# Performance work log

Measured on AMD Instinct MI355X. Metric: run time of the kernel, lower is better.

The kernel has to match this reference:

```python
import jax, jax.numpy as jnp
import numpy as np

N = 50000   # nodes
E = 200000  # edges
C = 32      # conv_dim
ND = 75     # n_atom_features
ED = 12     # n_bond_features
L = 3       # num_layer
G = 500     # num graphs in batch
HID = 5     # neurons_message
EPS = 1e-5


def leaky(v):
    return jnp.where(v > 0, v, 0.01 * v)


def setup_inputs() -> dict:
    key = jax.random.key(0)
    ks = jax.random.split(key, 16)
    x = jax.random.normal(ks[0], (N, ND), jnp.float32)
    edge_index = jax.random.randint(ks[1], (2, E), 0, N, jnp.int32)
    edge_attr = jax.random.uniform(ks[2], (E, ED), jnp.float32)
    batch = jnp.sort(jax.random.randint(ks[3], (N,), 0, G, jnp.int32))
    return {
        "x": x,
        "edge_index": edge_index,
        "edge_attr": edge_attr,
        "batch": batch,
        "lin_W": jax.random.normal(ks[4], (ND, C), jnp.float32) * 0.1,
        "lin_b": jnp.zeros((C,), jnp.float32),
        "mes_W1": jax.random.normal(ks[5], (L, ED, HID), jnp.float32) * 0.3,
        "mes_b1": jnp.zeros((L, HID), jnp.float32),
        "mes_W2": jax.random.normal(ks[6], (L, HID, C * C), jnp.float32) * 0.05,
        "mes_b2": jnp.zeros((L, C * C), jnp.float32),
        "root_W": jax.random.normal(ks[7], (L, C, C), jnp.float32) * 0.1,
        "conv_b": jnp.zeros((L, C), jnp.float32),
        "bn_g": jnp.ones((L, C), jnp.float32),
        "bn_b": jnp.zeros((L, C), jnp.float32),
        "pred_W": jax.random.normal(ks[8], (C, 1), jnp.float32) * 0.1,
        "pred_b": jnp.zeros((1,), jnp.float32),
    }


def reference(x, edge_index, edge_attr, batch, lin_W, lin_b, mes_W1, mes_b1,
              mes_W2, mes_b2, root_W, conv_b, bn_g, bn_b, pred_W, pred_b):
    src, dst = edge_index[0], edge_index[1]
    # initial atom projection
    h = leaky(x @ lin_W + lin_b)  # [N, C]
    for l in range(L):
        # edge MLP -> per-edge weight matrix [E, C, C]
        w = jnp.maximum(edge_attr @ mes_W1[l] + mes_b1[l], 0.0)
        w = (w @ mes_W2[l] + mes_b2[l]).reshape(E, C, C)
        # gather source features, per-edge matmul, scatter-add to targets
        msg = jnp.einsum('ec,ecd->ed', h[src], w)  # [E, C]
        agg = jax.ops.segment_sum(msg, dst, num_segments=N)  # [N, C]
        out = agg + h @ root_W[l] + conv_b[l]
        # batch norm (batch statistics over nodes)
        mu = out.mean(axis=0)
        var = out.var(axis=0)
        out = (out - mu) / jnp.sqrt(var + EPS) * bn_g[l] + bn_b[l]
        if l < L - 1:
            out = leaky(out)
        h = out  # JK == 'last'
    # graph readout: scatter_add over batch ids, then prediction head
    g = jax.ops.segment_sum(h, batch, num_segments=G)  # [G, C]
    return g @ pred_W + pred_b  # [G, 1]
```

## Files before the change

### kernel.cpp

```cpp
#include <hip/hip_runtime.h>

namespace {

constexpr int kN = 50000, kE = 200000, kG = 500;
constexpr float kEps = 1e-5f;

typedef short v8s __attribute__((ext_vector_type(8)));
typedef float v4f __attribute__((ext_vector_type(4)));

__device__ __forceinline__ unsigned short bf16rn(float x) {
    unsigned u = __float_as_uint(x);
    return (unsigned short)((u + 0x7FFFu + ((u >> 16) & 1u)) >> 16);
}
__device__ __forceinline__ float bf16lo(unsigned p) { return __uint_as_float(p << 16); }
__device__ __forceinline__ float bf16hi(unsigned p) { return __uint_as_float(p & 0xFFFF0000u); }
__device__ __forceinline__ unsigned pk2(float a, float b) {
    return (unsigned)bf16rn(a) | ((unsigned)bf16rn(b) << 16);
}

__global__ __launch_bounds__(1024) void init_h(
    const float* __restrict__ x, const float* __restrict__ W,
    const float* __restrict__ b, unsigned short* __restrict__ h16)
{
    __shared__ unsigned short sx[256 * 96];
    __shared__ unsigned short sW[32 * 96];
    int t = threadIdx.x;
    for (int i = t; i < 256 * 96; i += 1024) sx[i] = 0;
    for (int i = t; i < 32 * 96; i += 1024) sW[i] = 0;
    __syncthreads();
    int tb = blockIdx.x * 256;
    int cnt = min(256, kN - tb);
    for (int i = t; i < cnt * 75; i += 1024) {
        int n = i / 75, f = i - n * 75;
        sx[n * 96 + f] = bf16rn(x[(size_t)tb * 75 + i]);
    }
    for (int i = t; i < 75 * 32; i += 1024) {
        int f = i >> 5, c = i & 31;
        sW[c * 96 + f] = bf16rn(W[i]);
    }
    __syncthreads();
    int l15 = t & 15, quad = (t >> 4) & 3, w = t >> 6;
    int n = tb + w * 16 + l15;
    unsigned* H = (unsigned*)h16;
    #pragma unroll
    for (int tile = 0; tile < 2; ++tile) {
        v4f acc = {0.f, 0.f, 0.f, 0.f};
        #pragma unroll
        for (int kc = 0; kc < 3; ++kc) {
            v8s a  = *(const v8s*)&sW[(tile * 16 + l15) * 96 + kc * 32 + quad * 8];
            v8s bb = *(const v8s*)&sx[(w * 16 + l15) * 96 + kc * 32 + quad * 8];
            acc = __builtin_amdgcn_mfma_f32_16x16x32_bf16(a, bb, acc, 0, 0, 0);
        }
        if (n < kN) {
            int c0 = tile * 16 + quad * 4;
            float v0 = acc[0] + b[c0],     v1 = acc[1] + b[c0 + 1];
            float v2 = acc[2] + b[c0 + 2], v3 = acc[3] + b[c0 + 3];
            v0 = v0 > 0.f ? v0 : 0.01f * v0;  v1 = v1 > 0.f ? v1 : 0.01f * v1;
            v2 = v2 > 0.f ? v2 : 0.01f * v2;  v3 = v3 > 0.f ? v3 : 0.01f * v3;
            H[n * 16 + (c0 >> 1)]     = pk2(v0, v1);
            H[n * 16 + (c0 >> 1) + 1] = pk2(v2, v3);
        }
    }
}

__global__ __launch_bounds__(256) void hid_pre(
    const float* __restrict__ ea, const float* __restrict__ W1,
    const float* __restrict__ b1, unsigned* __restrict__ hidpk)
{
    __shared__ float sE[256 * 13];
    __shared__ float sW[195];
    int t = threadIdx.x;
    for (int i = t; i < 195; i += 256) sW[i] = (i < 180) ? W1[i] : b1[i - 180];
    int base = blockIdx.x * 256;
    int cnt = min(256, kE - base);
    for (int i = t; i < cnt * 12; i += 256) {
        int el = i / 12, f = i - el * 12;
        sE[el * 13 + f] = ea[(size_t)base * 12 + i];
    }
    __syncthreads();
    if (t >= cnt) return;
    int e = base + t;
    float ef[12];
    #pragma unroll
    for (int j = 0; j < 12; ++j) ef[j] = sE[t * 13 + j];
    #pragma unroll
    for (int l = 0; l < 3; ++l) {
        float h[5];
        #pragma unroll
        for (int k = 0; k < 5; ++k) h[k] = sW[180 + l * 5 + k];
        #pragma unroll
        for (int f = 0; f < 12; ++f)
            #pragma unroll
            for (int k = 0; k < 5; ++k)
                h[k] = fmaf(ef[f], sW[l * 60 + f * 5 + k], h[k]);
        #pragma unroll
        for (int k = 0; k < 5; ++k) h[k] = h[k] > 0.f ? h[k] : 0.f;
        size_t o = ((size_t)l * kE + e) * 3;
        hidpk[o + 0] = pk2(h[0], h[1]);
        hidpk[o + 1] = pk2(h[2], h[3]);
        hidpk[o + 2] = pk2(h[4], 0.f);
    }
}

__global__ __launch_bounds__(1024) void y_root(
    const unsigned short* __restrict__ h16, float* __restrict__ obuf,
    const float* __restrict__ W2, const float* __restrict__ b2,
    const float* __restrict__ rW, const float* __restrict__ convb,
    const float* __restrict__ stats,
    const float* __restrict__ gPrev, const float* __restrict__ bPrev,
    int first, unsigned short* __restrict__ Yus)
{
    __shared__ unsigned short sh[256 * 32];
    __shared__ unsigned short sB[256 * 32];
    int t = threadIdx.x;
    int tb = blockIdx.x * 256;
    int cnt = min(256, kN - tb);
    for (int i = t; i < 8192; i += 1024) {
        int co = i >> 5, c = i & 31, d = co >> 3, k = co & 7;
        float v = (k < 5) ? W2[k * 1024 + c * 32 + d]
                : (k == 5) ? b2[c * 32 + d]
                : (k == 6) ? rW[c * 32 + d] : 0.f;
        sB[co * 32 + c] = bf16rn(v);
    }
    if (first) {
        #pragma unroll
        for (int j = 0; j < 8; ++j) {
            int idx = t + j * 1024;
            int nl = idx >> 5, c = idx & 31;
            sh[idx] = (nl < cnt) ? h16[(size_t)(tb + nl) * 32 + c] : (unsigned short)0;
        }
    } else {
        int c = t & 31;
        float mu = stats[c] * (1.f / kN);
        float var = stats[32 + c] * (1.f / kN) - mu * mu;
        float ivg = rsqrtf(var + kEps) * gPrev[c];
        float bb = bPrev[c];
        #pragma unroll
        for (int j = 0; j < 8; ++j) {
            int idx = t + j * 1024;
            int nl = idx >> 5;
            float v = 0.f;
            if (nl < cnt) {
                float o = obuf[(size_t)(tb + nl) * 32 + c];
                v = (o - mu) * ivg + bb;
                v = v > 0.f ? v : 0.01f * v;
            }
            sh[idx] = bf16rn(v);
        }
    }
    __syncthreads();
    int l15 = t & 15, quad = (t >> 4) & 3, w = t >> 6;
    int n = tb + w * 16 + l15;
    v8s bn_ = *(const v8s*)&sh[(w * 16 + l15) * 32 + quad * 8];
    unsigned* Ydw = (unsigned*)Yus;
    #pragma unroll
    for (int i = 0; i < 16; ++i) {
        v8s a = *(const v8s*)&sB[(i * 16 + l15) * 32 + quad * 8];
        v4f acc = {0.f, 0.f, 0.f, 0.f};
        acc = __builtin_amdgcn_mfma_f32_16x16x32_bf16(a, bn_, acc, 0, 0, 0);
        if (n < kN) {
            int cb = i * 16 + quad * 4;
            int d = cb >> 3, koff = cb & 7;
            if (koff == 0) {
                Ydw[(size_t)n * 128 + d * 4]     = pk2(acc[0], acc[1]);
                Ydw[(size_t)n * 128 + d * 4 + 1] = pk2(acc[2], acc[3]);
            } else {
                Ydw[(size_t)n * 128 + d * 4 + 2] = pk2(acc[0], acc[1]);
                obuf[(size_t)n * 32 + d] = acc[2] + convb[d];
            }
        }
    }
}

__global__ __launch_bounds__(256) void edge_msg(
    const int* __restrict__ ei, const unsigned* __restrict__ hp,
    const unsigned short* __restrict__ Yus, float* __restrict__ obuf,
    float* __restrict__ stats)
{
    int t = threadIdx.x;
    if (blockIdx.x == 0 && t < 64) stats[t] = 0.f;
    int gid = blockIdx.x * 256 + t;
    int e = gid >> 5, d = gid & 31;
    int src = ei[e];
    int dst = ei[kE + e];
    unsigned q0 = hp[(size_t)e * 3 + 0];
    unsigned q1 = hp[(size_t)e * 3 + 1];
    unsigned q2 = hp[(size_t)e * 3 + 2];
    uint4 p = *(const uint4*)(Yus + (size_t)src * 256 + d * 8);
    float m = bf16hi(p.z);
    m = fmaf(bf16lo(q0), bf16lo(p.x), m);
    m = fmaf(bf16hi(q0), bf16hi(p.x), m);
    m = fmaf(bf16lo(q1), bf16lo(p.y), m);
    m = fmaf(bf16hi(q1), bf16hi(p.y), m);
    m = fmaf(bf16lo(q2), bf16lo(p.z), m);
    atomicAdd(&obuf[(size_t)dst * 32 + d], m);
}

__global__ __launch_bounds__(256) void bn_reduce(
    const float* __restrict__ obuf, float* __restrict__ stats)
{
    __shared__ float ls[256];
    __shared__ float lq[256];
    int t = threadIdx.x;
    int c = t & 31, row = t >> 5;
    float s = 0.f, q = 0.f;
    for (int n = blockIdx.x * 8 + row; n < kN; n += gridDim.x * 8) {
        float v = obuf[(size_t)n * 32 + c];
        s += v; q += v * v;
    }
    ls[t] = s; lq[t] = q;
    __syncthreads();
    if (t < 128) { ls[t] += ls[t + 128]; lq[t] += lq[t + 128]; }
    __syncthreads();
    if (t < 64) { ls[t] += ls[t + 64]; lq[t] += lq[t + 64]; }
    __syncthreads();
    if (t < 32) {
        atomicAdd(&stats[t], ls[t] + ls[t + 32]);
        atomicAdd(&stats[32 + t], lq[t] + lq[t + 32]);
    }
}

__global__ __launch_bounds__(256) void bn_norm_final(
    const float* __restrict__ obuf, const float* __restrict__ stats,
    const float* __restrict__ g, const float* __restrict__ b,
    float* __restrict__ vbuf, const float* __restrict__ predW,
    float* __restrict__ out, const float* __restrict__ pred_b)
{
    int idx = blockIdx.x * 256 + threadIdx.x;
    if (idx < kG) out[idx] = pred_b[0];
    if (idx >= kN * 32) return;
    int c = idx & 31;
    float mu = stats[c] * (1.f / kN);
    float var = stats[32 + c] * (1.f / kN) - mu * mu;
    float inv = rsqrtf(var + kEps);
    float v = (obuf[idx] - mu) * inv * g[c] + b[c];
    float pv = v * predW[c];
    #pragma unroll
    for (int off = 16; off > 0; off >>= 1) pv += __shfl_down(pv, off, 32);
    if (c == 0) vbuf[idx >> 5] = pv;
}

__global__ __launch_bounds__(256) void seg_readout(
    const float* __restrict__ vbuf, const int* __restrict__ batch,
    float* __restrict__ out)
{
    __shared__ float ls[kG];
    int t = threadIdx.x;
    for (int i = t; i < kG; i += 256) ls[i] = 0.f;
    __syncthreads();
    int base = blockIdx.x * 2048 + t * 8;
    int cur = -1; float acc = 0.f;
    #pragma unroll
    for (int i = 0; i < 8; ++i) {
        int n = base + i;
        if (n >= kN) break;
        int gi = batch[n];
        float val = vbuf[n];
        if (gi != cur) {
            if (cur >= 0) atomicAdd(&ls[cur], acc);
            cur = gi; acc = val;
        } else acc += val;
    }
    if (cur >= 0) atomicAdd(&ls[cur], acc);
    __syncthreads();
    for (int i = t; i < kG; i += 256) {
        float s = ls[i];
        if (s != 0.f) atomicAdd(&out[i], s);
    }
}

}

extern "C" void kernel_launch(void* const* d_in, const int* in_sizes, int n_in,
                              void* d_out, int out_size, void* d_ws, size_t ws_size,
                              hipStream_t stream)
{
    const float* x      = (const float*)d_in[0];
    const int*   ei     = (const int*)d_in[1];
    const float* ea     = (const float*)d_in[2];
    const int*   batch  = (const int*)d_in[3];
    const float* lin_W  = (const float*)d_in[4];
    const float* lin_b  = (const float*)d_in[5];
    const float* mes_W1 = (const float*)d_in[6];
    const float* mes_b1 = (const float*)d_in[7];
    const float* mes_W2 = (const float*)d_in[8];
    const float* mes_b2 = (const float*)d_in[9];
    const float* root_W = (const float*)d_in[10];
    const float* conv_b = (const float*)d_in[11];
    const float* bn_g   = (const float*)d_in[12];
    const float* bn_b   = (const float*)d_in[13];
    const float* pred_W = (const float*)d_in[14];
    const float* pred_b = (const float*)d_in[15];
    float* out = (float*)d_out;

    char* wsb = (char*)d_ws;
    float* stats = (float*)wsb;
    unsigned short* h16 = (unsigned short*)(wsb + 256);
    float* obuf = (float*)(h16 + (size_t)kN * 32);
    unsigned short* Yus = (unsigned short*)(obuf + (size_t)kN * 32);
    unsigned* hidpk = (unsigned*)(Yus + (size_t)kN * 256);
    float* vbuf = (float*)Yus;

    init_h<<<(kN + 255) / 256, 1024, 0, stream>>>(x, lin_W, lin_b, h16);
    hid_pre<<<(kE + 255) / 256, 256, 0, stream>>>(ea, mes_W1, mes_b1, hidpk);

    for (int l = 0; l < 3; ++l) {
        y_root<<<(kN + 255) / 256, 1024, 0, stream>>>(
            h16, obuf, mes_W2 + (size_t)l * 5120, mes_b2 + (size_t)l * 1024,
            root_W + (size_t)l * 1024, conv_b + l * 32, stats,
            bn_g + (l ? (l - 1) * 32 : 0), bn_b + (l ? (l - 1) * 32 : 0),
            l == 0 ? 1 : 0, Yus);
        edge_msg<<<kE * 32 / 256, 256, 0, stream>>>(
            ei, hidpk + (size_t)l * kE * 3, Yus, obuf, stats);
        bn_reduce<<<512, 256, 0, stream>>>(obuf, stats);
    }

    bn_norm_final<<<(kN * 32 + 255) / 256, 256, 0, stream>>>(
        obuf, stats, bn_g + 64, bn_b + 64, vbuf, pred_W, out, pred_b);
    seg_readout<<<(kN + 2047) / 2048, 256, 0, stream>>>(vbuf, batch, out);
}
```

Before: 310.2 us.

## Replace atomic edge scatter with CSR pull aggregation fused with BN statistics

Builds a destination-sorted CSR (degree count, single-block scan, atomic fill) once per call. The per-layer atomic edge_msg scatter and separate bn_reduce pass are replaced by a pull-style agg kernel that sums incoming messages per node and accumulates BN statistics in the same pass. It also switches the per-node Y and h buffers from bf16 to fp32 in a k-major layout and gives each layer its own stats slice. This removes the float atomics and one full obuf read per layer, at the cost of CSR build kernels, a serial single-block scan, doubled Y storage traffic, and load imbalance across node degrees.

```diff
diff --git a/kernel.cpp b/kernel.cpp
--- a/kernel.cpp
+++ b/kernel.cpp
@@ -18,9 +18,16 @@
     return (unsigned)bf16rn(a) | ((unsigned)bf16rn(b) << 16);
 }
 
+__global__ __launch_bounds__(256) void zero_init(int* __restrict__ deg,
+                                                 float* __restrict__ stats) {
+    int i = blockIdx.x * 256 + threadIdx.x;
+    if (i < kN) deg[i] = 0;
+    if (i < 192) stats[i] = 0.f;
+}
+
 __global__ __launch_bounds__(1024) void init_h(
     const float* __restrict__ x, const float* __restrict__ W,
-    const float* __restrict__ b, unsigned short* __restrict__ h16)
+    const float* __restrict__ b, float* __restrict__ hbuf)
 {
     __shared__ unsigned short sx[256 * 96];
     __shared__ unsigned short sW[32 * 96];
@@ -40,32 +47,32 @@
     }
     __syncthreads();
     int l15 = t & 15, quad = (t >> 4) & 3, w = t >> 6;
-    int n = tb + w * 16 + l15;
-    unsigned* H = (unsigned*)h16;
     #pragma unroll
     for (int tile = 0; tile < 2; ++tile) {
         v4f acc = {0.f, 0.f, 0.f, 0.f};
         #pragma unroll
         for (int kc = 0; kc < 3; ++kc) {
-            v8s a  = *(const v8s*)&sW[(tile * 16 + l15) * 96 + kc * 32 + quad * 8];
-            v8s bb = *(const v8s*)&sx[(w * 16 + l15) * 96 + kc * 32 + quad * 8];
+            v8s a  = *(const v8s*)&sx[(w * 16 + l15) * 96 + kc * 32 + quad * 8];
+            v8s bb = *(const v8s*)&sW[(tile * 16 + l15) * 96 + kc * 32 + quad * 8];
             acc = __builtin_amdgcn_mfma_f32_16x16x32_bf16(a, bb, acc, 0, 0, 0);
         }
-        if (n < kN) {
-            int c0 = tile * 16 + quad * 4;
-            float v0 = acc[0] + b[c0],     v1 = acc[1] + b[c0 + 1];
-            float v2 = acc[2] + b[c0 + 2], v3 = acc[3] + b[c0 + 3];
-            v0 = v0 > 0.f ? v0 : 0.01f * v0;  v1 = v1 > 0.f ? v1 : 0.01f * v1;
-            v2 = v2 > 0.f ? v2 : 0.01f * v2;  v3 = v3 > 0.f ? v3 : 0.01f * v3;
-            H[n * 16 + (c0 >> 1)]     = pk2(v0, v1);
-            H[n * 16 + (c0 >> 1) + 1] = pk2(v2, v3);
+        int c = tile * 16 + l15;
+        float bc = b[c];
+        #pragma unroll
+        for (int r = 0; r < 4; ++r) {
+            int n = tb + w * 16 + quad * 4 + r;
+            if (n < kN) {
+                float v = acc[r] + bc;
+                hbuf[(size_t)n * 32 + c] = v > 0.f ? v : 0.01f * v;
+            }
         }
     }
 }
 
 __global__ __launch_bounds__(256) void hid_pre(
     const float* __restrict__ ea, const float* __restrict__ W1,
-    const float* __restrict__ b1, unsigned* __restrict__ hidpk)
+    const float* __restrict__ b1, const int* __restrict__ ei,
+    unsigned* __restrict__ hidpk, int* __restrict__ deg)
 {
     __shared__ float sE[256 * 13];
     __shared__ float sW[195];
@@ -80,6 +87,7 @@
     __syncthreads();
     if (t >= cnt) return;
     int e = base + t;
+    atomicAdd(&deg[ei[kE + e]], 1);
     float ef[12];
     #pragma unroll
     for (int j = 0; j < 12; ++j) ef[j] = sE[t * 13 + j];
@@ -102,24 +110,68 @@
     }
 }
 
+__global__ __launch_bounds__(1024) void csr_scan(
+    const int* __restrict__ deg, int* __restrict__ rowptr,
+    int* __restrict__ cursor)
+{
+    __shared__ int sc[1024];
+    const int C = 49;
+    int t = threadIdx.x;
+    int base = t * C;
+    int s = 0;
+    for (int i = 0; i < C; ++i) {
+        int idx = base + i;
+        if (idx < kN) s += deg[idx];
+    }
+    sc[t] = s;
+    __syncthreads();
+    for (int off = 1; off < 1024; off <<= 1) {
+        int v = (t >= off) ? sc[t - off] : 0;
+        __syncthreads();
+        sc[t] += v;
+        __syncthreads();
+    }
+    int p = sc[t] - s;
+    for (int i = 0; i < C; ++i) {
+        int idx = base + i;
+        if (idx < kN) {
+            rowptr[idx] = p;
+            cursor[idx] = p;
+            p += deg[idx];
+        }
+    }
+    if (t == 1023) rowptr[kN] = p;
+}
+
+__global__ __launch_bounds__(256) void csr_fill(
+    const int* __restrict__ ei, int* __restrict__ cursor,
+    int* __restrict__ csr_src, int* __restrict__ csr_eid)
+{
+    int e = blockIdx.x * 256 + threadIdx.x;
+    if (e >= kE) return;
+    int dst = ei[kE + e];
+    int pos = atomicAdd(&cursor[dst], 1);
+    csr_src[pos] = ei[e];
+    csr_eid[pos] = e;
+}
+
 __global__ __launch_bounds__(1024) void y_root(
-    const unsigned short* __restrict__ h16, float* __restrict__ obuf,
+    const float* __restrict__ hbuf, float* __restrict__ obuf,
     const float* __restrict__ W2, const float* __restrict__ b2,
     const float* __restrict__ rW, const float* __restrict__ convb,
     const float* __restrict__ stats,
     const float* __restrict__ gPrev, const float* __restrict__ bPrev,
-    int first, unsigned short* __restrict__ Yus)
+    int first, float* __restrict__ Yf)
 {
     __shared__ unsigned short sh[256 * 32];
-    __shared__ unsigned short sB[256 * 32];
+    __shared__ unsigned short sB[224 * 32];
     int t = threadIdx.x;
     int tb = blockIdx.x * 256;
     int cnt = min(256, kN - tb);
-    for (int i = t; i < 8192; i += 1024) {
-        int co = i >> 5, c = i & 31, d = co >> 3, k = co & 7;
+    for (int i = t; i < 224 * 32; i += 1024) {
+        int co = i >> 5, c = i & 31, k = co >> 5, d = co & 31;
         float v = (k < 5) ? W2[k * 1024 + c * 32 + d]
-                : (k == 5) ? b2[c * 32 + d]
-                : (k == 6) ? rW[c * 32 + d] : 0.f;
+                : (k == 5) ? b2[c * 32 + d] : rW[c * 32 + d];
         sB[co * 32 + c] = bf16rn(v);
     }
     if (first) {
@@ -127,7 +179,8 @@
         for (int j = 0; j < 8; ++j) {
             int idx = t + j * 1024;
             int nl = idx >> 5, c = idx & 31;
-            sh[idx] = (nl < cnt) ? h16[(size_t)(tb + nl) * 32 + c] : (unsigned short)0;
+            float v = (nl < cnt) ? hbuf[(size_t)(tb + nl) * 32 + c] : 0.f;
+            sh[idx] = bf16rn(v);
         }
     } else {
         int c = t & 31;
@@ -150,64 +203,65 @@
     }
     __syncthreads();
     int l15 = t & 15, quad = (t >> 4) & 3, w = t >> 6;
-    int n = tb + w * 16 + l15;
-    v8s bn_ = *(const v8s*)&sh[(w * 16 + l15) * 32 + quad * 8];
-    unsigned* Ydw = (unsigned*)Yus;
-    #pragma unroll
-    for (int i = 0; i < 16; ++i) {
-        v8s a = *(const v8s*)&sB[(i * 16 + l15) * 32 + quad * 8];
+    v8s a = *(const v8s*)&sh[(w * 16 + l15) * 32 + quad * 8];
+    #pragma unroll
+    for (int i = 0; i < 14; ++i) {
+        v8s bb = *(const v8s*)&sB[(i * 16 + l15) * 32 + quad * 8];
         v4f acc = {0.f, 0.f, 0.f, 0.f};
-        acc = __builtin_amdgcn_mfma_f32_16x16x32_bf16(a, bn_, acc, 0, 0, 0);
-        if (n < kN) {
-            int cb = i * 16 + quad * 4;
-            int d = cb >> 3, koff = cb & 7;
-            if (koff == 0) {
-                Ydw[(size_t)n * 128 + d * 4]     = pk2(acc[0], acc[1]);
-                Ydw[(size_t)n * 128 + d * 4 + 1] = pk2(acc[2], acc[3]);
-            } else {
-                Ydw[(size_t)n * 128 + d * 4 + 2] = pk2(acc[0], acc[1]);
-                obuf[(size_t)n * 32 + d] = acc[2] + convb[d];
+        acc = __builtin_amdgcn_mfma_f32_16x16x32_bf16(a, bb, acc, 0, 0, 0);
+        int co = i * 16 + l15, k = co >> 5, d = co & 31;
+        if (k < 6) {
+            #pragma unroll
+            for (int r = 0; r < 4; ++r) {
+                int n = tb + w * 16 + quad * 4 + r;
+                if (n < kN) Yf[(size_t)n * 192 + k * 32 + d] = acc[r];
             }
-        }
-    }
-}
-
-__global__ __launch_bounds__(256) void edge_msg(
-    const int* __restrict__ ei, const unsigned* __restrict__ hp,
-    const unsigned short* __restrict__ Yus, float* __restrict__ obuf,
-    float* __restrict__ stats)
-{
-    int t = threadIdx.x;
-    if (blockIdx.x == 0 && t < 64) stats[t] = 0.f;
-    int gid = blockIdx.x * 256 + t;
-    int e = gid >> 5, d = gid & 31;
-    int src = ei[e];
-    int dst = ei[kE + e];
-    unsigned q0 = hp[(size_t)e * 3 + 0];
-    unsigned q1 = hp[(size_t)e * 3 + 1];
-    unsigned q2 = hp[(size_t)e * 3 + 2];
-    uint4 p = *(const uint4*)(Yus + (size_t)src * 256 + d * 8);
-    float m = bf16hi(p.z);
-    m = fmaf(bf16lo(q0), bf16lo(p.x), m);
-    m = fmaf(bf16hi(q0), bf16hi(p.x), m);
-    m = fmaf(bf16lo(q1), bf16lo(p.y), m);
-    m = fmaf(bf16hi(q1), bf16hi(p.y), m);
-    m = fmaf(bf16lo(q2), bf16lo(p.z), m);
-    atomicAdd(&obuf[(size_t)dst * 32 + d], m);
-}
-
-__global__ __launch_bounds__(256) void bn_reduce(
-    const float* __restrict__ obuf, float* __restrict__ stats)
-{
+        } else {
+            float cb = convb[d];
+            #pragma unroll
+            for (int r = 0; r < 4; ++r) {
+                int n = tb + w * 16 + quad * 4 + r;
+                if (n < kN) obuf[(size_t)n * 32 + d] = acc[r] + cb;
+            }
+        }
+    }
+}
+
+__global__ __launch_bounds__(256) void agg(
+    const int* __restrict__ rowptr, const int* __restrict__ csr_src,
+    const int* __restrict__ csr_eid, const unsigned* __restrict__ hp,
+    const float* __restrict__ Yf, float* __restrict__ obuf,
+    float* __restrict__ statsL)
+{
+    int t = threadIdx.x;
+    int grp = t >> 5, d = t & 31;
+    int nbase = blockIdx.x * 64 + grp * 8;
+    float s = 0.f, q = 0.f;
+    for (int ii = 0; ii < 8; ++ii) {
+        int n = nbase + ii;
+        if (n >= kN) break;
+        float acc = obuf[(size_t)n * 32 + d];
+        int j0 = rowptr[n], j1 = rowptr[n + 1];
+        for (int j = j0; j < j1; ++j) {
+            int src = csr_src[j];
+            int eid = csr_eid[j];
+            unsigned q0 = hp[(size_t)eid * 3 + 0];
+            unsigned q1 = hp[(size_t)eid * 3 + 1];
+            unsigned q2 = hp[(size_t)eid * 3 + 2];
+            const float* yr = Yf + (size_t)src * 192;
+            float m = yr[160 + d];
+            m = fmaf(bf16lo(q0), yr[d], m);
+            m = fmaf(bf16hi(q0), yr[32 + d], m);
+            m = fmaf(bf16lo(q1), yr[64 + d], m);
+            m = fmaf(bf16hi(q1), yr[96 + d], m);
+            m = fmaf(bf16lo(q2), yr[128 + d], m);
+            acc += m;
+        }
+        obuf[(size_t)n * 32 + d] = acc;
+        s += acc; q += acc * acc;
+    }
     __shared__ float ls[256];
     __shared__ float lq[256];
-    int t = threadIdx.x;
-    int c = t & 31, row = t >> 5;
-    float s = 0.f, q = 0.f;
-    for (int n = blockIdx.x * 8 + row; n < kN; n += gridDim.x * 8) {
-        float v = obuf[(size_t)n * 32 + c];
-        s += v; q += v * v;
-    }
     ls[t] = s; lq[t] = q;
     __syncthreads();
     if (t < 128) { ls[t] += ls[t + 128]; lq[t] += lq[t + 128]; }
@@ -215,8 +269,8 @@
     if (t < 64) { ls[t] += ls[t + 64]; lq[t] += lq[t + 64]; }
     __syncthreads();
     if (t < 32) {
-        atomicAdd(&stats[t], ls[t] + ls[t + 32]);
-        atomicAdd(&stats[32 + t], lq[t] + lq[t + 32]);
+        atomicAdd(&statsL[t], ls[t] + ls[t + 32]);
+        atomicAdd(&statsL[32 + t], lq[t] + lq[t + 32]);
     }
 }
 
@@ -294,28 +348,37 @@
     float* out = (float*)d_out;
 
     char* wsb = (char*)d_ws;
-    float* stats = (float*)wsb;
-    unsigned short* h16 = (unsigned short*)(wsb + 256);
-    float* obuf = (float*)(h16 + (size_t)kN * 32);
-    unsigned short* Yus = (unsigned short*)(obuf + (size_t)kN * 32);
-    unsigned* hidpk = (unsigned*)(Yus + (size_t)kN * 256);
-    float* vbuf = (float*)Yus;
-
-    init_h<<<(kN + 255) / 256, 1024, 0, stream>>>(x, lin_W, lin_b, h16);
-    hid_pre<<<(kE + 255) / 256, 256, 0, stream>>>(ea, mes_W1, mes_b1, hidpk);
+    float* stats   = (float*)wsb;
+    int* deg       = (int*)(wsb + 1024);
+    int* rowptr    = deg + kN;
+    int* cursor    = rowptr + kN + 1;
+    int* csr_src   = cursor + kN;
+    int* csr_eid   = csr_src + kE;
+    float* hbuf    = (float*)(csr_eid + kE);
+    float* obuf    = hbuf + (size_t)kN * 32;
+    float* Yf      = obuf + (size_t)kN * 32;
+    unsigned* hidpk = (unsigned*)(Yf + (size_t)kN * 192);
+    float* vbuf    = Yf;
+
+    zero_init<<<(kN + 255) / 256, 256, 0, stream>>>(deg, stats);
+    init_h<<<(kN + 255) / 256, 1024, 0, stream>>>(x, lin_W, lin_b, hbuf);
+    hid_pre<<<(kE + 255) / 256, 256, 0, stream>>>(ea, mes_W1, mes_b1, ei, hidpk, deg);
+    csr_scan<<<1, 1024, 0, stream>>>(deg, rowptr, cursor);
+    csr_fill<<<(kE + 255) / 256, 256, 0, stream>>>(ei, cursor, csr_src, csr_eid);
 
     for (int l = 0; l < 3; ++l) {
         y_root<<<(kN + 255) / 256, 1024, 0, stream>>>(
-            h16, obuf, mes_W2 + (size_t)l * 5120, mes_b2 + (size_t)l * 1024,
-            root_W + (size_t)l * 1024, conv_b + l * 32, stats,
+            hbuf, obuf, mes_W2 + (size_t)l * 5120, mes_b2 + (size_t)l * 1024,
+            root_W + (size_t)l * 1024, conv_b + l * 32,
+            stats + (l ? (l - 1) * 64 : 0),
             bn_g + (l ? (l - 1) * 32 : 0), bn_b + (l ? (l - 1) * 32 : 0),
-            l == 0 ? 1 : 0, Yus);
-        edge_msg<<<kE * 32 / 256, 256, 0, stream>>>(
-            ei, hidpk + (size_t)l * kE * 3, Yus, obuf, stats);
-        bn_reduce<<<512, 256, 0, stream>>>(obuf, stats);
+            l == 0 ? 1 : 0, Yf);
+        agg<<<(kN + 63) / 64, 256, 0, stream>>>(
+            rowptr, csr_src, csr_eid, hidpk + (size_t)l * kE * 3, Yf, obuf,
+            stats + l * 64);
     }
 
     bn_norm_final<<<(kN * 32 + 255) / 256, 256, 0, stream>>>(
-        obuf, stats, bn_g + 64, bn_b + 64, vbuf, pred_W, out, pred_b);
+        obuf, stats + 128, bn_g + 64, bn_b + 64, vbuf, pred_W, out, pred_b);
     seg_readout<<<(kN + 2047) / 2048, 256, 0, stream>>>(vbuf, batch, out);
 }
```

New measurement: 471.8 us. 52.1% more time.

## Compute edge messages with per-edge MFMA instead of precomputed per-node Y tensor

Applied to the files above, without the earlier changes.

Drops the per-node Y expansion of size N×256 bf16, which every edge then gathered at 512 bytes per edge. Each edge block now gathers only the 64-byte h[src] row and runs MFMAs against the W2/b2 slices in shared memory, weighting the results by the edge hidden activations before atomically scattering to dst. src/dst indices are packed with the hidden values into one uint4 per edge. The BN stat accumulators are spread over 8 replicas per layer to cut atomic contention. The trade is much less memory traffic for more MFMA work per edge and a weight-staging step in every edge block.

```diff
diff --git a/kernel.cpp b/kernel.cpp
--- a/kernel.cpp
+++ b/kernel.cpp
@@ -4,6 +4,8 @@
 
 constexpr int kN = 50000, kE = 200000, kG = 500;
 constexpr float kEps = 1e-5f;
+constexpr int kNB = (kN + 255) / 256;
+constexpr int kEB = (kE + 255) / 256;
 
 typedef short v8s __attribute__((ext_vector_type(8)));
 typedef float v4f __attribute__((ext_vector_type(4)));
@@ -65,7 +67,8 @@
 
 __global__ __launch_bounds__(256) void hid_pre(
     const float* __restrict__ ea, const float* __restrict__ W1,
-    const float* __restrict__ b1, unsigned* __restrict__ hidpk)
+    const float* __restrict__ b1, const int* __restrict__ ei,
+    uint4* __restrict__ hq)
 {
     __shared__ float sE[256 * 13];
     __shared__ float sW[195];
@@ -80,6 +83,8 @@
     __syncthreads();
     if (t >= cnt) return;
     int e = base + t;
+    unsigned src = (unsigned)ei[e];
+    unsigned dst = (unsigned)ei[kE + e];
     float ef[12];
     #pragma unroll
     for (int j = 0; j < 12; ++j) ef[j] = sE[t * 13 + j];
@@ -95,109 +100,153 @@
                 h[k] = fmaf(ef[f], sW[l * 60 + f * 5 + k], h[k]);
         #pragma unroll
         for (int k = 0; k < 5; ++k) h[k] = h[k] > 0.f ? h[k] : 0.f;
-        size_t o = ((size_t)l * kE + e) * 3;
-        hidpk[o + 0] = pk2(h[0], h[1]);
-        hidpk[o + 1] = pk2(h[2], h[3]);
-        hidpk[o + 2] = pk2(h[4], 0.f);
-    }
-}
-
-__global__ __launch_bounds__(1024) void y_root(
-    const unsigned short* __restrict__ h16, float* __restrict__ obuf,
-    const float* __restrict__ W2, const float* __restrict__ b2,
+        hq[(size_t)l * kE + e] = make_uint4(
+            pk2(h[0], h[1]), pk2(h[2], h[3]),
+            (unsigned)bf16rn(h[4]) | (src << 16), dst);
+    }
+}
+
+__global__ __launch_bounds__(256) void norm_root(
+    const float* __restrict__ obuf_prev, unsigned short* __restrict__ h16,
+    float* __restrict__ obuf,
     const float* __restrict__ rW, const float* __restrict__ convb,
-    const float* __restrict__ stats,
+    const float* __restrict__ statsR,
     const float* __restrict__ gPrev, const float* __restrict__ bPrev,
-    int first, unsigned short* __restrict__ Yus)
+    int first)
 {
     __shared__ unsigned short sh[256 * 32];
-    __shared__ unsigned short sB[256 * 32];
+    __shared__ unsigned short sR[32 * 32];
     int t = threadIdx.x;
     int tb = blockIdx.x * 256;
     int cnt = min(256, kN - tb);
-    for (int i = t; i < 8192; i += 1024) {
-        int co = i >> 5, c = i & 31, d = co >> 3, k = co & 7;
-        float v = (k < 5) ? W2[k * 1024 + c * 32 + d]
-                : (k == 5) ? b2[c * 32 + d]
-                : (k == 6) ? rW[c * 32 + d] : 0.f;
-        sB[co * 32 + c] = bf16rn(v);
+    for (int i = t; i < 1024; i += 256) {
+        int d = i >> 5, c = i & 31;
+        sR[d * 32 + c] = bf16rn(rW[c * 32 + d]);
     }
     if (first) {
         #pragma unroll
-        for (int j = 0; j < 8; ++j) {
-            int idx = t + j * 1024;
-            int nl = idx >> 5, c = idx & 31;
-            sh[idx] = (nl < cnt) ? h16[(size_t)(tb + nl) * 32 + c] : (unsigned short)0;
+        for (int j = 0; j < 4; ++j) {
+            int i4 = t + j * 256;
+            int nl = i4 >> 2, part = i4 & 3;
+            uint4 v = make_uint4(0, 0, 0, 0);
+            if (nl < cnt)
+                v = ((const uint4*)(h16 + (size_t)(tb + nl) * 32))[part];
+            ((uint4*)sh)[i4] = v;
         }
     } else {
         int c = t & 31;
-        float mu = stats[c] * (1.f / kN);
-        float var = stats[32 + c] * (1.f / kN) - mu * mu;
+        float sum = 0.f, sq = 0.f;
+        #pragma unroll
+        for (int r = 0; r < 8; ++r) {
+            sum += statsR[r * 64 + c];
+            sq  += statsR[r * 64 + 32 + c];
+        }
+        float mu = sum * (1.f / kN);
+        float var = sq * (1.f / kN) - mu * mu;
         float ivg = rsqrtf(var + kEps) * gPrev[c];
         float bb = bPrev[c];
-        #pragma unroll
-        for (int j = 0; j < 8; ++j) {
-            int idx = t + j * 1024;
+        for (int j = 0; j < 32; ++j) {
+            int idx = t + j * 256;
             int nl = idx >> 5;
             float v = 0.f;
             if (nl < cnt) {
-                float o = obuf[(size_t)(tb + nl) * 32 + c];
+                float o = obuf_prev[(size_t)(tb + nl) * 32 + c];
                 v = (o - mu) * ivg + bb;
                 v = v > 0.f ? v : 0.01f * v;
+                h16[(size_t)(tb + nl) * 32 + c] = bf16rn(v);
             }
             sh[idx] = bf16rn(v);
         }
     }
     __syncthreads();
     int l15 = t & 15, quad = (t >> 4) & 3, w = t >> 6;
-    int n = tb + w * 16 + l15;
-    v8s bn_ = *(const v8s*)&sh[(w * 16 + l15) * 32 + quad * 8];
-    unsigned* Ydw = (unsigned*)Yus;
-    #pragma unroll
-    for (int i = 0; i < 16; ++i) {
-        v8s a = *(const v8s*)&sB[(i * 16 + l15) * 32 + quad * 8];
-        v4f acc = {0.f, 0.f, 0.f, 0.f};
-        acc = __builtin_amdgcn_mfma_f32_16x16x32_bf16(a, bn_, acc, 0, 0, 0);
-        if (n < kN) {
-            int cb = i * 16 + quad * 4;
-            int d = cb >> 3, koff = cb & 7;
-            if (koff == 0) {
-                Ydw[(size_t)n * 128 + d * 4]     = pk2(acc[0], acc[1]);
-                Ydw[(size_t)n * 128 + d * 4 + 1] = pk2(acc[2], acc[3]);
-            } else {
-                Ydw[(size_t)n * 128 + d * 4 + 2] = pk2(acc[0], acc[1]);
-                obuf[(size_t)n * 32 + d] = acc[2] + convb[d];
+    #pragma unroll
+    for (int jt = 0; jt < 4; ++jt) {
+        int nl = w * 64 + jt * 16 + l15;
+        v8s bfrag = *(const v8s*)&sh[nl * 32 + quad * 8];
+        #pragma unroll
+        for (int i = 0; i < 2; ++i) {
+            v8s a = *(const v8s*)&sR[(i * 16 + l15) * 32 + quad * 8];
+            v4f acc = {0.f, 0.f, 0.f, 0.f};
+            acc = __builtin_amdgcn_mfma_f32_16x16x32_bf16(a, bfrag, acc, 0, 0, 0);
+            if (nl < cnt) {
+                #pragma unroll
+                for (int r = 0; r < 4; ++r) {
+                    int d = i * 16 + quad * 4 + r;
+                    obuf[(size_t)(tb + nl) * 32 + d] = acc[r] + convb[d];
+                }
             }
         }
     }
 }
 
-__global__ __launch_bounds__(256) void edge_msg(
-    const int* __restrict__ ei, const unsigned* __restrict__ hp,
-    const unsigned short* __restrict__ Yus, float* __restrict__ obuf,
-    float* __restrict__ stats)
-{
-    int t = threadIdx.x;
-    if (blockIdx.x == 0 && t < 64) stats[t] = 0.f;
-    int gid = blockIdx.x * 256 + t;
-    int e = gid >> 5, d = gid & 31;
-    int src = ei[e];
-    int dst = ei[kE + e];
-    unsigned q0 = hp[(size_t)e * 3 + 0];
-    unsigned q1 = hp[(size_t)e * 3 + 1];
-    unsigned q2 = hp[(size_t)e * 3 + 2];
-    uint4 p = *(const uint4*)(Yus + (size_t)src * 256 + d * 8);
-    float m = bf16hi(p.z);
-    m = fmaf(bf16lo(q0), bf16lo(p.x), m);
-    m = fmaf(bf16hi(q0), bf16hi(p.x), m);
-    m = fmaf(bf16lo(q1), bf16lo(p.y), m);
-    m = fmaf(bf16hi(q1), bf16hi(p.y), m);
-    m = fmaf(bf16lo(q2), bf16lo(p.z), m);
-    atomicAdd(&obuf[(size_t)dst * 32 + d], m);
+__global__ __launch_bounds__(256) void edge_mfma(
+    const uint4* __restrict__ hq, const unsigned short* __restrict__ h16,
+    const float* __restrict__ W2, const float* __restrict__ b2,
+    float* __restrict__ obuf, float* __restrict__ statsL)
+{
+    __shared__ unsigned short sB[192 * 32];
+    __shared__ unsigned short sh[256 * 32];
+    __shared__ uint4 sq[256];
+    int t = threadIdx.x;
+    if (blockIdx.x == 0)
+        for (int i = t; i < 512; i += 256) statsL[i] = 0.f;
+    int base = blockIdx.x * 256;
+    int cnt = min(256, kE - base);
+    for (int i = t; i < 192 * 32; i += 256) {
+        int co = i >> 5, c = i & 31, k = co >> 5, d = co & 31;
+        float v = (k < 5) ? W2[k * 1024 + c * 32 + d] : b2[c * 32 + d];
+        sB[co * 32 + c] = bf16rn(v);
+    }
+    sq[t] = (t < cnt) ? hq[base + t] : make_uint4(0, 0, 0, 0);
+    __syncthreads();
+    #pragma unroll
+    for (int pass = 0; pass < 4; ++pass) {
+        int e = pass * 64 + (t >> 2);
+        int l4 = t & 3;
+        uint4 v = make_uint4(0, 0, 0, 0);
+        if (e < cnt) {
+            unsigned src = sq[e].z >> 16;
+            v = ((const uint4*)(h16 + (size_t)src * 32))[l4];
+        }
+        ((uint4*)(sh + e * 32))[l4] = v;
+    }
+    __syncthreads();
+    int l15 = t & 15, quad = (t >> 4) & 3, w = t >> 6;
+    #pragma unroll 2
+    for (int jt = 0; jt < 4; ++jt) {
+        int el = w * 64 + jt * 16 + l15;
+        uint4 qq = sq[el];
+        float hk[6];
+        hk[0] = bf16lo(qq.x); hk[1] = bf16hi(qq.x);
+        hk[2] = bf16lo(qq.y); hk[3] = bf16hi(qq.y);
+        hk[4] = bf16lo(qq.z); hk[5] = 1.f;
+        int dst = (int)qq.w;
+        v8s bfrag = *(const v8s*)&sh[el * 32 + quad * 8];
+        float macc[2][4] = {{0.f,0.f,0.f,0.f},{0.f,0.f,0.f,0.f}};
+        #pragma unroll
+        for (int i = 0; i < 12; ++i) {
+            v8s a = *(const v8s*)&sB[(i * 16 + l15) * 32 + quad * 8];
+            v4f acc = {0.f, 0.f, 0.f, 0.f};
+            acc = __builtin_amdgcn_mfma_f32_16x16x32_bf16(a, bfrag, acc, 0, 0, 0);
+            float hv = hk[i >> 1];
+            int half = i & 1;
+            #pragma unroll
+            for (int r = 0; r < 4; ++r)
+                macc[half][r] = fmaf(hv, acc[r], macc[half][r]);
+        }
+        #pragma unroll
+        for (int half = 0; half < 2; ++half)
+            #pragma unroll
+            for (int r = 0; r < 4; ++r) {
+                int d = half * 16 + quad * 4 + r;
+                atomicAdd(&obuf[(size_t)dst * 32 + d], macc[half][r]);
+            }
+    }
 }
 
 __global__ __launch_bounds__(256) void bn_reduce(
-    const float* __restrict__ obuf, float* __restrict__ stats)
+    const float* __restrict__ obuf, float* __restrict__ statsR)
 {
     __shared__ float ls[256];
     __shared__ float lq[256];
@@ -215,13 +264,14 @@
     if (t < 64) { ls[t] += ls[t + 64]; lq[t] += lq[t + 64]; }
     __syncthreads();
     if (t < 32) {
-        atomicAdd(&stats[t], ls[t] + ls[t + 32]);
-        atomicAdd(&stats[32 + t], lq[t] + lq[t + 32]);
+        float* rep = statsR + (blockIdx.x & 7) * 64;
+        atomicAdd(&rep[t], ls[t] + ls[t + 32]);
+        atomicAdd(&rep[32 + t], lq[t] + lq[t + 32]);
     }
 }
 
 __global__ __launch_bounds__(256) void bn_norm_final(
-    const float* __restrict__ obuf, const float* __restrict__ stats,
+    const float* __restrict__ obuf, const float* __restrict__ statsR,
     const float* __restrict__ g, const float* __restrict__ b,
     float* __restrict__ vbuf, const float* __restrict__ predW,
     float* __restrict__ out, const float* __restrict__ pred_b)
@@ -230,8 +280,14 @@
     if (idx < kG) out[idx] = pred_b[0];
     if (idx >= kN * 32) return;
     int c = idx & 31;
-    float mu = stats[c] * (1.f / kN);
-    float var = stats[32 + c] * (1.f / kN) - mu * mu;
+    float sum = 0.f, sq = 0.f;
+    #pragma unroll
+    for (int r = 0; r < 8; ++r) {
+        sum += statsR[r * 64 + c];
+        sq  += statsR[r * 64 + 32 + c];
+    }
+    float mu = sum * (1.f / kN);
+    float var = sq * (1.f / kN) - mu * mu;
     float inv = rsqrtf(var + kEps);
     float v = (obuf[idx] - mu) * inv * g[c] + b[c];
     float pv = v * predW[c];
@@ -295,27 +351,28 @@
 
     char* wsb = (char*)d_ws;
     float* stats = (float*)wsb;
-    unsigned short* h16 = (unsigned short*)(wsb + 256);
+    unsigned short* h16 = (unsigned short*)(wsb + 8192);
     float* obuf = (float*)(h16 + (size_t)kN * 32);
-    unsigned short* Yus = (unsigned short*)(obuf + (size_t)kN * 32);
-    unsigned* hidpk = (unsigned*)(Yus + (size_t)kN * 256);
-    float* vbuf = (float*)Yus;
-
-    init_h<<<(kN + 255) / 256, 1024, 0, stream>>>(x, lin_W, lin_b, h16);
-    hid_pre<<<(kE + 255) / 256, 256, 0, stream>>>(ea, mes_W1, mes_b1, hidpk);
+    uint4* hq   = (uint4*)(obuf + (size_t)kN * 32);
+    float* vbuf = (float*)h16;
+
+    init_h<<<kNB, 1024, 0, stream>>>(x, lin_W, lin_b, h16);
+    hid_pre<<<kEB, 256, 0, stream>>>(ea, mes_W1, mes_b1, ei, hq);
 
     for (int l = 0; l < 3; ++l) {
-        y_root<<<(kN + 255) / 256, 1024, 0, stream>>>(
-            h16, obuf, mes_W2 + (size_t)l * 5120, mes_b2 + (size_t)l * 1024,
-            root_W + (size_t)l * 1024, conv_b + l * 32, stats,
+        norm_root<<<kNB, 256, 0, stream>>>(
+            obuf, h16, obuf, root_W + (size_t)l * 1024, conv_b + l * 32,
+            stats + (l ? (l - 1) * 512 : 0),
             bn_g + (l ? (l - 1) * 32 : 0), bn_b + (l ? (l - 1) * 32 : 0),
-            l == 0 ? 1 : 0, Yus);
-        edge_msg<<<kE * 32 / 256, 256, 0, stream>>>(
-            ei, hidpk + (size_t)l * kE * 3, Yus, obuf, stats);
-        bn_reduce<<<512, 256, 0, stream>>>(obuf, stats);
+            l == 0 ? 1 : 0);
+        edge_mfma<<<kEB, 256, 0, stream>>>(
+            hq + (size_t)l * kE, h16,
+            mes_W2 + (size_t)l * 5120, mes_b2 + (size_t)l * 1024,
+            obuf, stats + l * 512);
+        bn_reduce<<<512, 256, 0, stream>>>(obuf, stats + l * 512);
     }
 
     bn_norm_final<<<(kN * 32 + 255) / 256, 256, 0, stream>>>(
-        obuf, stats, bn_g + 64, bn_b + 64, vbuf, pred_W, out, pred_b);
+        obuf, stats + 2 * 512, bn_g + 64, bn_b + 64, vbuf, pred_W, out, pred_b);
     seg_readout<<<(kN + 2047) / 2048, 256, 0, stream>>>(vbuf, batch, out);
 }
```

Measured after the change: 635.7 us. +104.9%, slower.
